# Kernel optimization log

Measured on AMD Instinct MI355X. Metric: run time of the kernel, lower is better.

## Reference

```python
import jax, jax.numpy as jnp
import numpy as np

N = 100000
E = 1000000
IN_DIM = 64
OUT_DIM = 64


def setup_inputs() -> dict:
    key = jax.random.key(0)
    k1, k2, k3, k4 = jax.random.split(key, 4)
    x = jax.random.normal(k1, (N, IN_DIM), dtype=jnp.float32)
    edge_index = jax.random.randint(k2, (2, E), 0, N, dtype=jnp.int64)
    # nn.Linear(in_dim, out_dim): weight (out,in), bias (out,)
    bound = 1.0 / np.sqrt(IN_DIM)
    W = jax.random.uniform(k3, (OUT_DIM, IN_DIM), dtype=jnp.float32, minval=-bound, maxval=bound)
    b = jax.random.uniform(k4, (OUT_DIM,), dtype=jnp.float32, minval=-bound, maxval=bound)
    return {"x": x, "edge_index": edge_index, "W": W, "b": b}


def reference(x, edge_index, W, b):
    i = edge_index[0]  # target nodes (E,)
    j = edge_index[1]  # source nodes (E,)
    msg = x[j] @ W.T + b  # (E, out_dim)
    n = x.shape[0]
    out = jax.ops.segment_sum(msg, i, num_segments=n)  # (N, out_dim)
    deg = jax.ops.segment_sum(jnp.ones((i.shape[0],), dtype=msg.dtype), i, num_segments=n)
    deg = jnp.maximum(deg, 1.0)[:, None]
    return out / deg
```

## Files before the change

### kernel.cpp

```cpp
#include <hip/hip_runtime.h>

constexpr int N_NODES = 100000;
constexpr int N_EDGES = 1000000;
constexpr int DIM = 64;

constexpr int CAP  = 16;
constexpr int MAXO = 32768;

constexpr int TILE = 64;
constexpr int PAD  = 65;

__global__ __launch_bounds__(256) void build_slots(
    const int* __restrict__ eidx, int* __restrict__ cnt,
    int* __restrict__ noflow, int* __restrict__ oflow, int* __restrict__ slot)
{
    int e = blockIdx.x * 256 + threadIdx.x;
    if (e >= N_EDGES) return;
    int i = __builtin_nontemporal_load(eidx + e);
    int j = __builtin_nontemporal_load(eidx + N_EDGES + e);
    int pos = atomicAdd(&cnt[i], 1);
    if (pos < CAP) {
        slot[(i << 4) + pos] = j;
    } else {
        int o = atomicAdd(noflow, 1);
        if (o < MAXO) { oflow[2 * o] = i; oflow[2 * o + 1] = j; }
    }
}

__global__ __launch_bounds__(256) void fused_gather_mm(
    const float* __restrict__ x, const int* __restrict__ cnt,
    const int* __restrict__ slot,
    const float* __restrict__ W, const float* __restrict__ b,
    float* __restrict__ out)
{
    __shared__ float tile[TILE * PAD];

    const int base = blockIdx.x * TILE;
    const int lane = threadIdx.x & 63;
    const int wid  = threadIdx.x >> 6;
    const int grp  = lane >> 4;
    const int l16  = lane & 15;
    const int c4   = l16 << 2;

#pragma unroll
    for (int pack = 0; pack < 4; ++pack) {
        const int row    = wid * 16 + pack * 4 + grp;
        const int node   = base + row;
        const bool valid = (node < N_NODES);
        const int nclamp = valid ? node : 0;
        const int d_true = valid ? cnt[node] : 0;
        const int d      = (d_true < CAP) ? d_true : CAP;

        const int jrow = slot[(nclamp << 4) + l16];

        float sx = 0.0f, sy = 0.0f, sz = 0.0f, sw = 0.0f;
#pragma unroll
        for (int u = 0; u < CAP; ++u) {
            const int  ju = __shfl(jrow, (grp << 4) | u);
            const bool ok = (u < d);
            const int  jj = ok ? ju : 0;
            const float4 v = *reinterpret_cast<const float4*>(
                x + ((size_t)jj << 6) + c4);
            sx += ok ? v.x : 0.0f;
            sy += ok ? v.y : 0.0f;
            sz += ok ? v.z : 0.0f;
            sw += ok ? v.w : 0.0f;
        }

        const float inv = (d_true > 0) ? 1.0f / (float)d_true : 0.0f;
        const int tb = row * PAD + c4;
        tile[tb + 0] = sx * inv;
        tile[tb + 1] = sy * inv;
        tile[tb + 2] = sz * inv;
        tile[tb + 3] = sw * inv;
    }
    __syncthreads();

    const int nd  = threadIdx.x & 63;
    const int d0u = __builtin_amdgcn_readfirstlane((threadIdx.x >> 6) << 4);
    const float* __restrict__ Wr = W + (size_t)d0u * DIM;

    float acc[16];
#pragma unroll
    for (int q = 0; q < 16; ++q) acc[q] = 0.0f;

#pragma unroll 4
    for (int k = 0; k < DIM; ++k) {
        float a = tile[nd * PAD + k];
#pragma unroll
        for (int q = 0; q < 16; ++q)
            acc[q] = fmaf(a, Wr[(size_t)q * DIM + k], acc[q]);
    }

    int gnode = base + nd;
    int dg = (gnode < N_NODES) ? cnt[gnode] : 0;
    __syncthreads();
#pragma unroll
    for (int q = 0; q < 16; ++q) {
        float v = (dg > 0) ? (acc[q] + b[d0u + q]) : 0.0f;
        tile[nd * PAD + d0u + q] = v;
    }
    __syncthreads();

#pragma unroll
    for (int r = 0; r < 16; ++r) {
        int idx = r * 256 + threadIdx.x;
        int row = idx >> 6, d = idx & 63;
        int g = base + row;
        if (g < N_NODES)
            out[(size_t)g * DIM + d] = tile[row * PAD + d];
    }
}

__global__ __launch_bounds__(256) void fixup_overflow(
    const int* __restrict__ noflow, const int* __restrict__ oflow,
    const int* __restrict__ cnt, const float* __restrict__ x,
    const float* __restrict__ W, float* __restrict__ out)
{
    int m = *noflow;
    if (m > MAXO) m = MAXO;
    const int lane = threadIdx.x & 63;
    const int wv   = (blockIdx.x * 256 + threadIdx.x) >> 6;
    const int nwv  = (gridDim.x * 256) >> 6;
    const float* __restrict__ wr = W + ((size_t)lane << 6);
    for (int o = wv; o < m; o += nwv) {
        const int i = oflow[2 * o];
        const int j = oflow[2 * o + 1];
        const float inv = 1.0f / (float)cnt[i];
        const float* __restrict__ xr = x + ((size_t)j << 6);
        float acc = 0.0f;
#pragma unroll
        for (int k4 = 0; k4 < 16; ++k4) {
            const float4 xv = *reinterpret_cast<const float4*>(xr + 4 * k4);
            const float4 wv4 = *reinterpret_cast<const float4*>(wr + 4 * k4);
            acc = fmaf(xv.x, wv4.x, acc);
            acc = fmaf(xv.y, wv4.y, acc);
            acc = fmaf(xv.z, wv4.z, acc);
            acc = fmaf(xv.w, wv4.w, acc);
        }
        atomicAdd(&out[((size_t)i << 6) + lane], acc * inv);
    }
}

extern "C" void kernel_launch(void* const* d_in, const int* in_sizes, int n_in,
                              void* d_out, int out_size, void* d_ws, size_t ws_size,
                              hipStream_t stream) {
    const float* x  = (const float*)d_in[0];
    const int*   ei = (const int*)d_in[1];
    const float* W  = (const float*)d_in[2];
    const float* b  = (const float*)d_in[3];
    float* out = (float*)d_out;

    int* cnt    = (int*)d_ws;
    int* noflow = cnt + N_NODES;
    int* oflow  = noflow + 1;
    int* slot   = oflow + 2 * MAXO;

    hipMemsetAsync(cnt, 0, (N_NODES + 1) * sizeof(int), stream);

    build_slots<<<(N_EDGES + 255) / 256, 256, 0, stream>>>(
        ei, cnt, noflow, oflow, slot);
    fused_gather_mm<<<(N_NODES + TILE - 1) / TILE, 256, 0, stream>>>(
        x, cnt, slot, W, b, out);
    fixup_overflow<<<128, 256, 0, stream>>>(noflow, oflow, cnt, x, W, out);
}
```

Before: 230.6 us.

## Replace per-edge global atomics with LDS-binned bucket staging for CSR build

Edge binning now runs per 8192-edge chunk. Each workgroup builds an LDS histogram over 256-node buckets, scatters packed (local offset, source) pairs into LDS, then does one global atomic per bucket to reserve space in a fixed-capacity staging array. The gather kernel reads its bucket's staging segment, filters entries for its 64-node sub-tile, and builds per-node slot lists and degrees with LDS atomics, so the random global atomics and scattered slot writes go away. In exchange, every gather block scans its whole bucket (four times redundant), the bucket capacity is capped at 3584 with silent drops, and the packing assumes source indices fit in 17 bits.

```diff
diff --git a/kernel.cpp b/kernel.cpp
--- a/kernel.cpp
+++ b/kernel.cpp
@@ -4,40 +4,131 @@
 constexpr int N_EDGES = 1000000;
 constexpr int DIM = 64;
 
+constexpr int BNODES = 256;
+constexpr int NBUCK  = (N_NODES + BNODES - 1) / BNODES;
+constexpr int SCAP   = 3584;
+constexpr int CHUNK  = 8192;
+constexpr int NWG_A  = (N_EDGES + CHUNK - 1) / CHUNK;
+
 constexpr int CAP  = 16;
 constexpr int MAXO = 32768;
 
 constexpr int TILE = 64;
 constexpr int PAD  = 65;
 
-__global__ __launch_bounds__(256) void build_slots(
-    const int* __restrict__ eidx, int* __restrict__ cnt,
-    int* __restrict__ noflow, int* __restrict__ oflow, int* __restrict__ slot)
+__global__ __launch_bounds__(256) void bin_edges(
+    const int* __restrict__ eidx, int* __restrict__ gcur,
+    int* __restrict__ staging)
 {
-    int e = blockIdx.x * 256 + threadIdx.x;
-    if (e >= N_EDGES) return;
-    int i = __builtin_nontemporal_load(eidx + e);
-    int j = __builtin_nontemporal_load(eidx + N_EDGES + e);
-    int pos = atomicAdd(&cnt[i], 1);
-    if (pos < CAP) {
-        slot[(i << 4) + pos] = j;
-    } else {
-        int o = atomicAdd(noflow, 1);
-        if (o < MAXO) { oflow[2 * o] = i; oflow[2 * o + 1] = j; }
+    __shared__ int            sval[CHUNK];
+    __shared__ unsigned short sbkt[CHUNK];
+    __shared__ int hist[512];
+    __shared__ int base[512];
+    __shared__ int gbase[512];
+    __shared__ int ps[256];
+
+    const int tid = threadIdx.x;
+    const int e0  = blockIdx.x * CHUNK;
+    const int n   = (N_EDGES - e0 < CHUNK) ? (N_EDGES - e0) : CHUNK;
+
+    for (int t = tid; t < 512; t += 256) hist[t] = 0;
+    __syncthreads();
+
+    for (int t = tid; t < n; t += 256) {
+        int i = eidx[e0 + t];
+        atomicAdd(&hist[i >> 8], 1);
+    }
+    __syncthreads();
+
+    int h0 = hist[2 * tid], h1 = hist[2 * tid + 1];
+    int pv = h0 + h1;
+    ps[tid] = pv;
+    __syncthreads();
+    for (int d = 1; d < 256; d <<= 1) {
+        int t = (tid >= d) ? ps[tid - d] : 0;
+        __syncthreads();
+        ps[tid] += t;
+        __syncthreads();
+    }
+    int pex = ps[tid] - pv;
+    base[2 * tid]     = pex;
+    base[2 * tid + 1] = pex + h0;
+    hist[2 * tid]     = pex;
+    hist[2 * tid + 1] = pex + h0;
+    __syncthreads();
+
+    for (int t = tid; t < n; t += 256) {
+        int i  = eidx[e0 + t];
+        int j  = eidx[N_EDGES + e0 + t];
+        int bk = i >> 8;
+        int pos = atomicAdd(&hist[bk], 1);
+        sval[pos] = ((i & 255) << 17) | j;
+        sbkt[pos] = (unsigned short)bk;
+    }
+    __syncthreads();
+
+    for (int t = tid; t < 512; t += 256) {
+        int c = hist[t] - base[t];
+        gbase[t] = (c > 0) ? atomicAdd(&gcur[t], c) : 0;
+    }
+    __syncthreads();
+
+    for (int t = tid; t < n; t += 256) {
+        int bk = sbkt[t];
+        int dst = gbase[bk] + (t - base[bk]);
+        if (dst < SCAP)
+            staging[bk * SCAP + dst] = sval[t];
     }
 }
 
 __global__ __launch_bounds__(256) void fused_gather_mm(
-    const float* __restrict__ x, const int* __restrict__ cnt,
-    const int* __restrict__ slot,
+    const float* __restrict__ x, const int* __restrict__ gcur,
+    const int* __restrict__ staging,
     const float* __restrict__ W, const float* __restrict__ b,
-    float* __restrict__ out)
+    int* __restrict__ noflow, int* __restrict__ oflow,
+    int* __restrict__ deg_g, float* __restrict__ out)
 {
     __shared__ float tile[TILE * PAD];
-
+    __shared__ int   lds_slot[TILE * CAP];
+    __shared__ int   lcnt[TILE];
+
+    const int tid  = threadIdx.x;
     const int base = blockIdx.x * TILE;
-    const int lane = threadIdx.x & 63;
-    const int wid  = threadIdx.x >> 6;
+    const int bk   = blockIdx.x >> 2;
+    const int sub  = blockIdx.x & 3;
+
+    if (tid < TILE) lcnt[tid] = 0;
+    __syncthreads();
+
+    int m = gcur[bk];
+    if (m > SCAP) m = SCAP;
+    const int sg = bk * SCAP;
+    for (int t = tid; t < m; t += 256) {
+        int pk  = staging[sg + t];
+        int off = pk >> 17;
+        if ((off >> 6) == sub) {
+            int r = off & 63;
+            int pos = atomicAdd(&lcnt[r], 1);
+            if (pos < CAP) {
+                lds_slot[(r << 4) + pos] = pk & 0x1FFFF;
+            } else {
+                int o = atomicAdd(noflow, 1);
+                if (o < MAXO) {
+                    oflow[2 * o]     = (bk << 8) + off;
+                    oflow[2 * o + 1] = pk & 0x1FFFF;
+                }
+            }
+        }
+    }
+    __syncthreads();
+
+    if (tid < TILE) {
+        int g = base + tid;
+        if (g < N_NODES) deg_g[g] = lcnt[tid];
+    }
+
+    const int lane = tid & 63;
+    const int wid  = tid >> 6;
     const int grp  = lane >> 4;
     const int l16  = lane & 15;
     const int c4   = l16 << 2;
@@ -47,11 +138,10 @@
         const int row    = wid * 16 + pack * 4 + grp;
         const int node   = base + row;
         const bool valid = (node < N_NODES);
-        const int nclamp = valid ? node : 0;
-        const int d_true = valid ? cnt[node] : 0;
+        const int d_true = valid ? lcnt[row] : 0;
         const int d      = (d_true < CAP) ? d_true : CAP;
 
-        const int jrow = slot[(nclamp << 4) + l16];
+        const int jrow = lds_slot[(row << 4) + l16];
 
         float sx = 0.0f, sy = 0.0f, sz = 0.0f, sw = 0.0f;
 #pragma unroll
@@ -76,8 +166,8 @@
     }
     __syncthreads();
 
-    const int nd  = threadIdx.x & 63;
-    const int d0u = __builtin_amdgcn_readfirstlane((threadIdx.x >> 6) << 4);
+    const int nd  = tid & 63;
+    const int d0u = __builtin_amdgcn_readfirstlane((tid >> 6) << 4);
     const float* __restrict__ Wr = W + (size_t)d0u * DIM;
 
     float acc[16];
@@ -92,8 +182,7 @@
             acc[q] = fmaf(a, Wr[(size_t)q * DIM + k], acc[q]);
     }
 
-    int gnode = base + nd;
-    int dg = (gnode < N_NODES) ? cnt[gnode] : 0;
+    const int dg = lcnt[nd];
     __syncthreads();
 #pragma unroll
     for (int q = 0; q < 16; ++q) {
@@ -104,7 +193,7 @@
 
 #pragma unroll
     for (int r = 0; r < 16; ++r) {
-        int idx = r * 256 + threadIdx.x;
+        int idx = r * 256 + tid;
         int row = idx >> 6, d = idx & 63;
         int g = base + row;
         if (g < N_NODES)
@@ -114,7 +203,7 @@
 
 __global__ __launch_bounds__(256) void fixup_overflow(
     const int* __restrict__ noflow, const int* __restrict__ oflow,
-    const int* __restrict__ cnt, const float* __restrict__ x,
+    const int* __restrict__ deg_g, const float* __restrict__ x,
     const float* __restrict__ W, float* __restrict__ out)
 {
     int m = *noflow;
@@ -126,12 +215,12 @@
     for (int o = wv; o < m; o += nwv) {
         const int i = oflow[2 * o];
         const int j = oflow[2 * o + 1];
-        const float inv = 1.0f / (float)cnt[i];
+        const float inv = 1.0f / (float)deg_g[i];
         const float* __restrict__ xr = x + ((size_t)j << 6);
         float acc = 0.0f;
 #pragma unroll
         for (int k4 = 0; k4 < 16; ++k4) {
-            const float4 xv = *reinterpret_cast<const float4*>(xr + 4 * k4);
+            const float4 xv  = *reinterpret_cast<const float4*>(xr + 4 * k4);
             const float4 wv4 = *reinterpret_cast<const float4*>(wr + 4 * k4);
             acc = fmaf(xv.x, wv4.x, acc);
             acc = fmaf(xv.y, wv4.y, acc);
@@ -151,16 +240,16 @@
     const float* b  = (const float*)d_in[3];
     float* out = (float*)d_out;
 
-    int* cnt    = (int*)d_ws;
-    int* noflow = cnt + N_NODES;
-    int* oflow  = noflow + 1;
-    int* slot   = oflow + 2 * MAXO;
-
-    hipMemsetAsync(cnt, 0, (N_NODES + 1) * sizeof(int), stream);
-
-    build_slots<<<(N_EDGES + 255) / 256, 256, 0, stream>>>(
-        ei, cnt, noflow, oflow, slot);
+    int* gcur    = (int*)d_ws;
+    int* noflow  = gcur + NBUCK;
+    int* oflow   = noflow + 1;
+    int* deg_g   = oflow + 2 * MAXO;
+    int* staging = deg_g + N_NODES;
+
+    hipMemsetAsync(gcur, 0, (NBUCK + 1) * sizeof(int), stream);
+
+    bin_edges<<<NWG_A, 256, 0, stream>>>(ei, gcur, staging);
     fused_gather_mm<<<(N_NODES + TILE - 1) / TILE, 256, 0, stream>>>(
-        x, cnt, slot, W, b, out);
-    fixup_overflow<<<128, 256, 0, stream>>>(noflow, oflow, cnt, x, W, out);
-}
+        x, gcur, staging, W, b, noflow, oflow, deg_g, out);
+    fixup_overflow<<<128, 256, 0, stream>>>(noflow, oflow, deg_g, x, W, out);
+}
```

Measured after the change: 210.0 us. -8.9%, faster.
